# Kernel optimization log

Hardware: AMD Instinct MI355X
Metric: run time of the kernel (lower is better)

Reference implementation:

```python
import jax, jax.numpy as jnp
import numpy as np

B, W, F, N = 256, 512, 512, 512


def setup_inputs() -> dict:
    key = jax.random.key(0)
    k1, k2, k3, k4, k5 = jax.random.split(key, 5)
    return {
        "x": jax.random.normal(k1, (B, W, F), dtype=jnp.float32),
        "weight_k": jax.random.normal(k2, (F, N), dtype=jnp.float32),
        "weight_q": jax.random.normal(k3, (F, N), dtype=jnp.float32),
        "weight_v": jax.random.normal(k4, (F, N), dtype=jnp.float32),
        "w": jax.random.normal(k5, (W, 1), dtype=jnp.float32),
    }


def reference(x, weight_k, weight_q, weight_v, w):
    # x: (B, W, F)
    n_outputs = weight_k.shape[-1]
    # Per-word K/V projections (original loops over words; here one batched GEMM)
    K = jnp.einsum("bwf,fn->bwn", x, weight_k)  # (B, W, N)
    V = jnp.einsum("bwf,fn->bwn", x, weight_v)  # (B, W, N)
    # Per-sample query: t = x^T @ w -> (F,), q = t @ weight_q -> (N,)
    t = jnp.einsum("bwf,w->bf", x, w[:, 0])     # (B, F)
    Q = t @ weight_q                              # (B, N)
    # Scores over words, scaled, softmax across the word axis
    scores = jnp.einsum("bn,bwn->bw", Q, K) / jnp.sqrt(jnp.float32(n_outputs))
    weights = jax.nn.softmax(scores, axis=1)      # (B, W)
    # Weighted sum of V over words
    return jnp.einsum("bw,bwn->bn", weights, V)   # (B, N)
```

## Files before the change

kernel.cpp:

```cpp
#include <hip/hip_runtime.h>
#include <math.h>

#define B 256
#define W 512
#define F 512
#define N 512
#define GP 8
#define WPB (W / GP)

__global__ __launch_bounds__(256, 8) void tpart_kernel(
    const float* __restrict__ x,
    const float* __restrict__ wvec,
    float* __restrict__ t_part)
{
    const int blk  = blockIdx.x;
    const int g    = blk & (GP - 1);
    const int b    = blk >> 3;
    const int tid  = threadIdx.x;
    const int half = tid >> 7;
    const int f4   = tid & 127;

    __shared__ float s_w[WPB];
    __shared__ float s_part[2][F];

    if (tid < WPB) s_w[tid] = wvec[g * WPB + tid];
    __syncthreads();

    const float* xb = x + (size_t)b * W * F + (size_t)(g * WPB + half * 32) * F;
    float4 acc = make_float4(0.f, 0.f, 0.f, 0.f);
#pragma unroll 8
    for (int i = 0; i < 32; ++i) {
        const float4 xv = *(const float4*)(xb + (size_t)i * F + f4 * 4);
        const float  ww = s_w[half * 32 + i];
        acc.x += xv.x * ww; acc.y += xv.y * ww;
        acc.z += xv.z * ww; acc.w += xv.w * ww;
    }
    *(float4*)&s_part[half][f4 * 4] = acc;
    __syncthreads();

    t_part[(size_t)blk * F + tid]       = s_part[0][tid]       + s_part[1][tid];
    t_part[(size_t)blk * F + tid + 256] = s_part[0][tid + 256] + s_part[1][tid + 256];
}

__global__ __launch_bounds__(512) void qr_kernel(
    const float* __restrict__ t_part,
    const float* __restrict__ Wq,
    const float* __restrict__ Wk,
    float* __restrict__ r_out)
{
    __shared__ float s_t[F];
    __shared__ float s_q[N];
    const int b = blockIdx.x, tid = threadIdx.x;

    float t = 0.f;
#pragma unroll
    for (int g = 0; g < GP; ++g)
        t += t_part[((size_t)b * GP + g) * F + tid];
    s_t[tid] = t;
    __syncthreads();

    float qa[8] = {0.f, 0.f, 0.f, 0.f, 0.f, 0.f, 0.f, 0.f};
#pragma unroll 4
    for (int f = 0; f < F; f += 8) {
#pragma unroll
        for (int j = 0; j < 8; ++j)
            qa[j] += s_t[f + j] * Wq[(size_t)(f + j) * N + tid];
    }
    s_q[tid] = ((qa[0] + qa[1]) + (qa[2] + qa[3]))
             + ((qa[4] + qa[5]) + (qa[6] + qa[7]));
    __syncthreads();

    const float4* wkrow = (const float4*)(Wk + (size_t)tid * N);
    float r0 = 0.f, r1 = 0.f, r2 = 0.f, r3 = 0.f;
#pragma unroll 8
    for (int n4 = 0; n4 < N / 4; ++n4) {
        const float4 kv = wkrow[n4];
        const float4 qv = *(const float4*)&s_q[n4 * 4];
        r0 += kv.x * qv.x; r1 += kv.y * qv.y;
        r2 += kv.z * qv.z; r3 += kv.w * qv.w;
    }
    r_out[(size_t)b * F + tid] =
        ((r0 + r1) + (r2 + r3)) * 0.04419417382415922f;
}

__global__ __launch_bounds__(256, 6) void attn_part_kernel(
    const float* __restrict__ x,
    const float* __restrict__ r_in,
    float* __restrict__ c_part,
    float* __restrict__ ml_part)
{
    const int blk  = blockIdx.x;
    const int g    = blk & (GP - 1);
    const int b    = blk >> 3;
    const int tid  = threadIdx.x;
    const int lane = tid & 63;
    const int wv   = tid >> 6;

    __shared__ float s_c[4][F];
    __shared__ float s_m[4];
    __shared__ float s_l[4];

    const float* xb = x + (size_t)b * W * F;
    const float* rb = r_in + (size_t)b * F;
    const float4 r0 = *(const float4*)(rb + lane * 4);
    const float4 r1 = *(const float4*)(rb + 256 + lane * 4);

    float m = -INFINITY, l = 0.f;
    float4 c0 = make_float4(0.f, 0.f, 0.f, 0.f);
    float4 c1 = make_float4(0.f, 0.f, 0.f, 0.f);

    const int wbase = g * WPB + wv * 16;
#pragma unroll 2
    for (int i = 0; i < 16; i += 2) {
        const float* rowA = xb + (size_t)(wbase + i) * F;
        const float* rowB = rowA + F;
        const float4 a0 = *(const float4*)(rowA + lane * 4);
        const float4 a1 = *(const float4*)(rowA + 256 + lane * 4);
        const float4 b0 = *(const float4*)(rowB + lane * 4);
        const float4 b1 = *(const float4*)(rowB + 256 + lane * 4);

        float dA = a0.x * r0.x + a0.y * r0.y + a0.z * r0.z + a0.w * r0.w
                 + a1.x * r1.x + a1.y * r1.y + a1.z * r1.z + a1.w * r1.w;
        float dB = b0.x * r0.x + b0.y * r0.y + b0.z * r0.z + b0.w * r0.w
                 + b1.x * r1.x + b1.y * r1.y + b1.z * r1.z + b1.w * r1.w;
#pragma unroll
        for (int off = 32; off >= 1; off >>= 1) {
            dA += __shfl_xor(dA, off, 64);
            dB += __shfl_xor(dB, off, 64);
        }

        float mn = fmaxf(m, dA);
        float sc = __expf(m - mn);
        float p  = __expf(dA - mn);
        l = l * sc + p;
        c0.x = c0.x * sc + p * a0.x; c0.y = c0.y * sc + p * a0.y;
        c0.z = c0.z * sc + p * a0.z; c0.w = c0.w * sc + p * a0.w;
        c1.x = c1.x * sc + p * a1.x; c1.y = c1.y * sc + p * a1.y;
        c1.z = c1.z * sc + p * a1.z; c1.w = c1.w * sc + p * a1.w;
        m = mn;

        mn = fmaxf(m, dB);
        sc = __expf(m - mn);
        p  = __expf(dB - mn);
        l = l * sc + p;
        c0.x = c0.x * sc + p * b0.x; c0.y = c0.y * sc + p * b0.y;
        c0.z = c0.z * sc + p * b0.z; c0.w = c0.w * sc + p * b0.w;
        c1.x = c1.x * sc + p * b1.x; c1.y = c1.y * sc + p * b1.y;
        c1.z = c1.z * sc + p * b1.z; c1.w = c1.w * sc + p * b1.w;
        m = mn;
    }

    *(float4*)&s_c[wv][lane * 4]       = c0;
    *(float4*)&s_c[wv][256 + lane * 4] = c1;
    if (lane == 0) { s_m[wv] = m; s_l[wv] = l; }
    __syncthreads();

    float M = fmaxf(fmaxf(s_m[0], s_m[1]), fmaxf(s_m[2], s_m[3]));
    float a0w = __expf(s_m[0] - M), a1w = __expf(s_m[1] - M);
    float a2w = __expf(s_m[2] - M), a3w = __expf(s_m[3] - M);
    float L = a0w * s_l[0] + a1w * s_l[1] + a2w * s_l[2] + a3w * s_l[3];

#pragma unroll
    for (int k = 0; k < 2; ++k) {
        const int f = tid + k * 256;
        c_part[(size_t)blk * F + f] =
            a0w * s_c[0][f] + a1w * s_c[1][f] + a2w * s_c[2][f] + a3w * s_c[3][f];
    }
    if (tid == 0) { ml_part[blk * 2] = M; ml_part[blk * 2 + 1] = L; }
}

__global__ __launch_bounds__(512) void combine_kernel(
    const float* __restrict__ c_part,
    const float* __restrict__ ml_part,
    const float* __restrict__ Wv,
    float* __restrict__ out)
{
    __shared__ float s_cf[F];
    const int b = blockIdx.x, tid = threadIdx.x;

    float Mg[GP];
#pragma unroll
    for (int g = 0; g < GP; ++g) Mg[g] = ml_part[(b * GP + g) * 2];
    float M = -INFINITY;
#pragma unroll
    for (int g = 0; g < GP; ++g) M = fmaxf(M, Mg[g]);

    float L = 0.f;
    float alpha[GP];
#pragma unroll
    for (int g = 0; g < GP; ++g) {
        alpha[g] = __expf(Mg[g] - M);
        L += alpha[g] * ml_part[(b * GP + g) * 2 + 1];
    }
    const float invL = 1.f / L;

    float cf = 0.f;
#pragma unroll
    for (int g = 0; g < GP; ++g)
        cf += alpha[g] * c_part[((size_t)b * GP + g) * F + tid];
    s_cf[tid] = cf * invL;
    __syncthreads();

    float oa[8] = {0.f, 0.f, 0.f, 0.f, 0.f, 0.f, 0.f, 0.f};
#pragma unroll 4
    for (int f = 0; f < F; f += 8) {
#pragma unroll
        for (int j = 0; j < 8; ++j)
            oa[j] += s_cf[f + j] * Wv[(size_t)(f + j) * N + tid];
    }
    out[(size_t)b * N + tid] = ((oa[0] + oa[1]) + (oa[2] + oa[3]))
                             + ((oa[4] + oa[5]) + (oa[6] + oa[7]));
}

extern "C" void kernel_launch(void* const* d_in, const int* in_sizes, int n_in,
                              void* d_out, int out_size, void* d_ws, size_t ws_size,
                              hipStream_t stream)
{
    const float* x    = (const float*)d_in[0];
    const float* Wk   = (const float*)d_in[1];
    const float* Wq   = (const float*)d_in[2];
    const float* Wv   = (const float*)d_in[3];
    const float* wvec = (const float*)d_in[4];
    float* out     = (float*)d_out;
    float* t_part  = (float*)d_ws;
    float* r       = t_part + (size_t)B * GP * F;
    float* c_part  = r + (size_t)B * F;
    float* ml_part = c_part + (size_t)B * GP * F;

    tpart_kernel<<<B * GP, 256, 0, stream>>>(x, wvec, t_part);
    qr_kernel<<<B, 512, 0, stream>>>(t_part, Wq, Wk, r);
    attn_part_kernel<<<B * GP, 256, 0, stream>>>(x, r, c_part, ml_part);
    combine_kernel<<<B, 512, 0, stream>>>(c_part, ml_part, Wv, out);
}
```

Baseline: 491.8 us.

## Split online-softmax attention into separate score and weighted-sum kernels

Replaces the fused online-softmax attention kernel with a per-batch score kernel that computes full softmax probabilities, followed by a weighted-sum kernel over x chunks. The tpart kernel and the new cpart kernel batch eight row loads before accumulating, to increase memory-level parallelism. This removes the serial rescaling and shuffle-reduction chain per word, at the cost of an extra full read of x and a strided per-thread row access pattern in the score kernel. The occupancy hints in launch bounds are also dropped.

```diff
diff --git a/kernel.cpp b/kernel.cpp
--- a/kernel.cpp
+++ b/kernel.cpp
@@ -8,7 +8,7 @@
 #define GP 8
 #define WPB (W / GP)
 
-__global__ __launch_bounds__(256, 8) void tpart_kernel(
+__global__ __launch_bounds__(256) void tpart_kernel(
     const float* __restrict__ x,
     const float* __restrict__ wvec,
     float* __restrict__ t_part)
@@ -28,12 +28,19 @@
 
     const float* xb = x + (size_t)b * W * F + (size_t)(g * WPB + half * 32) * F;
     float4 acc = make_float4(0.f, 0.f, 0.f, 0.f);
-#pragma unroll 8
-    for (int i = 0; i < 32; ++i) {
-        const float4 xv = *(const float4*)(xb + (size_t)i * F + f4 * 4);
-        const float  ww = s_w[half * 32 + i];
-        acc.x += xv.x * ww; acc.y += xv.y * ww;
-        acc.z += xv.z * ww; acc.w += xv.w * ww;
+    for (int c = 0; c < 4; ++c) {
+        float wr[8];
+#pragma unroll
+        for (int j = 0; j < 8; ++j) wr[j] = s_w[half * 32 + c * 8 + j];
+        float4 xv[8];
+#pragma unroll
+        for (int j = 0; j < 8; ++j)
+            xv[j] = *(const float4*)(xb + (size_t)(c * 8 + j) * F + f4 * 4);
+#pragma unroll
+        for (int j = 0; j < 8; ++j) {
+            acc.x += xv[j].x * wr[j]; acc.y += xv[j].y * wr[j];
+            acc.z += xv[j].z * wr[j]; acc.w += xv[j].w * wr[j];
+        }
     }
     *(float4*)&s_part[half][f4 * 4] = acc;
     __syncthreads();
@@ -83,122 +90,122 @@
         ((r0 + r1) + (r2 + r3)) * 0.04419417382415922f;
 }
 
-__global__ __launch_bounds__(256, 6) void attn_part_kernel(
+__global__ __launch_bounds__(512) void score_kernel(
     const float* __restrict__ x,
     const float* __restrict__ r_in,
-    float* __restrict__ c_part,
-    float* __restrict__ ml_part)
+    float* __restrict__ p_out)
+{
+    const int b = blockIdx.x, tid = threadIdx.x;
+    const int lane = tid & 63, wv = tid >> 6;
+    __shared__ float s_r[F];
+    __shared__ float s_mred[8];
+    __shared__ float s_lred[8];
+
+    s_r[tid] = r_in[(size_t)b * F + tid];
+    __syncthreads();
+
+    const float* xrow = x + (size_t)b * W * F + (size_t)tid * F;
+    float4 acc[8];
+#pragma unroll
+    for (int k = 0; k < 8; ++k) acc[k] = make_float4(0.f, 0.f, 0.f, 0.f);
+
+    for (int i = 0; i < 16; ++i) {
+        float4 xv[8];
+#pragma unroll
+        for (int k = 0; k < 8; ++k)
+            xv[k] = *(const float4*)(xrow + k * 64 + i * 4);
+#pragma unroll
+        for (int k = 0; k < 8; ++k) {
+            const float4 rv = *(const float4*)(&s_r[k * 64 + i * 4]);
+            acc[k].x += xv[k].x * rv.x; acc[k].y += xv[k].y * rv.y;
+            acc[k].z += xv[k].z * rv.z; acc[k].w += xv[k].w * rv.w;
+        }
+    }
+    float4 a = acc[0];
+#pragma unroll
+    for (int k = 1; k < 8; ++k) {
+        a.x += acc[k].x; a.y += acc[k].y; a.z += acc[k].z; a.w += acc[k].w;
+    }
+    const float s = (a.x + a.y) + (a.z + a.w);
+
+    float mv = s;
+#pragma unroll
+    for (int off = 32; off >= 1; off >>= 1)
+        mv = fmaxf(mv, __shfl_xor(mv, off, 64));
+    if (lane == 0) s_mred[wv] = mv;
+    __syncthreads();
+    float M = s_mred[0];
+#pragma unroll
+    for (int j = 1; j < 8; ++j) M = fmaxf(M, s_mred[j]);
+
+    const float e = __expf(s - M);
+    float ls = e;
+#pragma unroll
+    for (int off = 32; off >= 1; off >>= 1)
+        ls += __shfl_xor(ls, off, 64);
+    if (lane == 0) s_lred[wv] = ls;
+    __syncthreads();
+    float L = 0.f;
+#pragma unroll
+    for (int j = 0; j < 8; ++j) L += s_lred[j];
+
+    p_out[(size_t)b * W + tid] = e / L;
+}
+
+__global__ __launch_bounds__(256) void cpart_kernel(
+    const float* __restrict__ x,
+    const float* __restrict__ p_in,
+    float* __restrict__ c_part)
 {
     const int blk  = blockIdx.x;
     const int g    = blk & (GP - 1);
     const int b    = blk >> 3;
     const int tid  = threadIdx.x;
-    const int lane = tid & 63;
-    const int wv   = tid >> 6;
-
-    __shared__ float s_c[4][F];
-    __shared__ float s_m[4];
-    __shared__ float s_l[4];
-
-    const float* xb = x + (size_t)b * W * F;
-    const float* rb = r_in + (size_t)b * F;
-    const float4 r0 = *(const float4*)(rb + lane * 4);
-    const float4 r1 = *(const float4*)(rb + 256 + lane * 4);
-
-    float m = -INFINITY, l = 0.f;
-    float4 c0 = make_float4(0.f, 0.f, 0.f, 0.f);
-    float4 c1 = make_float4(0.f, 0.f, 0.f, 0.f);
-
-    const int wbase = g * WPB + wv * 16;
-#pragma unroll 2
-    for (int i = 0; i < 16; i += 2) {
-        const float* rowA = xb + (size_t)(wbase + i) * F;
-        const float* rowB = rowA + F;
-        const float4 a0 = *(const float4*)(rowA + lane * 4);
-        const float4 a1 = *(const float4*)(rowA + 256 + lane * 4);
-        const float4 b0 = *(const float4*)(rowB + lane * 4);
-        const float4 b1 = *(const float4*)(rowB + 256 + lane * 4);
-
-        float dA = a0.x * r0.x + a0.y * r0.y + a0.z * r0.z + a0.w * r0.w
-                 + a1.x * r1.x + a1.y * r1.y + a1.z * r1.z + a1.w * r1.w;
-        float dB = b0.x * r0.x + b0.y * r0.y + b0.z * r0.z + b0.w * r0.w
-                 + b1.x * r1.x + b1.y * r1.y + b1.z * r1.z + b1.w * r1.w;
-#pragma unroll
-        for (int off = 32; off >= 1; off >>= 1) {
-            dA += __shfl_xor(dA, off, 64);
-            dB += __shfl_xor(dB, off, 64);
+    const int half = tid >> 7;
+    const int f4   = tid & 127;
+
+    __shared__ float s_p[WPB];
+    __shared__ float s_part[2][F];
+
+    if (tid < WPB) s_p[tid] = p_in[(size_t)b * W + g * WPB + tid];
+    __syncthreads();
+
+    const float* xb = x + (size_t)b * W * F + (size_t)(g * WPB + half * 32) * F;
+    float4 acc = make_float4(0.f, 0.f, 0.f, 0.f);
+    for (int c = 0; c < 4; ++c) {
+        float pr[8];
+#pragma unroll
+        for (int j = 0; j < 8; ++j) pr[j] = s_p[half * 32 + c * 8 + j];
+        float4 xv[8];
+#pragma unroll
+        for (int j = 0; j < 8; ++j)
+            xv[j] = *(const float4*)(xb + (size_t)(c * 8 + j) * F + f4 * 4);
+#pragma unroll
+        for (int j = 0; j < 8; ++j) {
+            acc.x += xv[j].x * pr[j]; acc.y += xv[j].y * pr[j];
+            acc.z += xv[j].z * pr[j]; acc.w += xv[j].w * pr[j];
         }
-
-        float mn = fmaxf(m, dA);
-        float sc = __expf(m - mn);
-        float p  = __expf(dA - mn);
-        l = l * sc + p;
-        c0.x = c0.x * sc + p * a0.x; c0.y = c0.y * sc + p * a0.y;
-        c0.z = c0.z * sc + p * a0.z; c0.w = c0.w * sc + p * a0.w;
-        c1.x = c1.x * sc + p * a1.x; c1.y = c1.y * sc + p * a1.y;
-        c1.z = c1.z * sc + p * a1.z; c1.w = c1.w * sc + p * a1.w;
-        m = mn;
-
-        mn = fmaxf(m, dB);
-        sc = __expf(m - mn);
-        p  = __expf(dB - mn);
-        l = l * sc + p;
-        c0.x = c0.x * sc + p * b0.x; c0.y = c0.y * sc + p * b0.y;
-        c0.z = c0.z * sc + p * b0.z; c0.w = c0.w * sc + p * b0.w;
-        c1.x = c1.x * sc + p * b1.x; c1.y = c1.y * sc + p * b1.y;
-        c1.z = c1.z * sc + p * b1.z; c1.w = c1.w * sc + p * b1.w;
-        m = mn;
-    }
-
-    *(float4*)&s_c[wv][lane * 4]       = c0;
-    *(float4*)&s_c[wv][256 + lane * 4] = c1;
-    if (lane == 0) { s_m[wv] = m; s_l[wv] = l; }
-    __syncthreads();
-
-    float M = fmaxf(fmaxf(s_m[0], s_m[1]), fmaxf(s_m[2], s_m[3]));
-    float a0w = __expf(s_m[0] - M), a1w = __expf(s_m[1] - M);
-    float a2w = __expf(s_m[2] - M), a3w = __expf(s_m[3] - M);
-    float L = a0w * s_l[0] + a1w * s_l[1] + a2w * s_l[2] + a3w * s_l[3];
-
-#pragma unroll
-    for (int k = 0; k < 2; ++k) {
-        const int f = tid + k * 256;
-        c_part[(size_t)blk * F + f] =
-            a0w * s_c[0][f] + a1w * s_c[1][f] + a2w * s_c[2][f] + a3w * s_c[3][f];
-    }
-    if (tid == 0) { ml_part[blk * 2] = M; ml_part[blk * 2 + 1] = L; }
+    }
+    *(float4*)&s_part[half][f4 * 4] = acc;
+    __syncthreads();
+
+    c_part[(size_t)blk * F + tid]       = s_part[0][tid]       + s_part[1][tid];
+    c_part[(size_t)blk * F + tid + 256] = s_part[0][tid + 256] + s_part[1][tid + 256];
 }
 
 __global__ __launch_bounds__(512) void combine_kernel(
     const float* __restrict__ c_part,
-    const float* __restrict__ ml_part,
     const float* __restrict__ Wv,
     float* __restrict__ out)
 {
     __shared__ float s_cf[F];
     const int b = blockIdx.x, tid = threadIdx.x;
 
-    float Mg[GP];
-#pragma unroll
-    for (int g = 0; g < GP; ++g) Mg[g] = ml_part[(b * GP + g) * 2];
-    float M = -INFINITY;
-#pragma unroll
-    for (int g = 0; g < GP; ++g) M = fmaxf(M, Mg[g]);
-
-    float L = 0.f;
-    float alpha[GP];
-#pragma unroll
-    for (int g = 0; g < GP; ++g) {
-        alpha[g] = __expf(Mg[g] - M);
-        L += alpha[g] * ml_part[(b * GP + g) * 2 + 1];
-    }
-    const float invL = 1.f / L;
-
     float cf = 0.f;
 #pragma unroll
     for (int g = 0; g < GP; ++g)
-        cf += alpha[g] * c_part[((size_t)b * GP + g) * F + tid];
-    s_cf[tid] = cf * invL;
+        cf += c_part[((size_t)b * GP + g) * F + tid];
+    s_cf[tid] = cf;
     __syncthreads();
 
     float oa[8] = {0.f, 0.f, 0.f, 0.f, 0.f, 0.f, 0.f, 0.f};
@@ -221,14 +228,15 @@
     const float* Wq   = (const float*)d_in[2];
     const float* Wv   = (const float*)d_in[3];
     const float* wvec = (const float*)d_in[4];
-    float* out     = (float*)d_out;
-    float* t_part  = (float*)d_ws;
-    float* r       = t_part + (size_t)B * GP * F;
-    float* c_part  = r + (size_t)B * F;
-    float* ml_part = c_part + (size_t)B * GP * F;
+    float* out    = (float*)d_out;
+    float* t_part = (float*)d_ws;
+    float* r      = t_part + (size_t)B * GP * F;
+    float* p      = r + (size_t)B * F;
+    float* c_part = p + (size_t)B * W;
 
     tpart_kernel<<<B * GP, 256, 0, stream>>>(x, wvec, t_part);
     qr_kernel<<<B, 512, 0, stream>>>(t_part, Wq, Wk, r);
-    attn_part_kernel<<<B * GP, 256, 0, stream>>>(x, r, c_part, ml_part);
-    combine_kernel<<<B, 512, 0, stream>>>(c_part, ml_part, Wv, out);
-}
+    score_kernel<<<B, 512, 0, stream>>>(x, r, p);
+    cpart_kernel<<<B * GP, 256, 0, stream>>>(x, p, c_part);
+    combine_kernel<<<B, 512, 0, stream>>>(c_part, Wv, out);
+}
```

New measurement: 755.9 us. +53.7%, slower.
